# Kernel tuning notes

Hardware: AMD Instinct MI355X
Metric: run time of the kernel (lower is better)

The kernel has to match this reference:

```python
import jax, jax.numpy as jnp
import numpy as np


def setup_inputs() -> dict:
    key = jax.random.key(0)
    k1, k2, k3 = jax.random.split(key, 3)
    D, L, BATCH = 768, 8192, 4
    h = jax.random.normal(k1, (D, L), dtype=jnp.float32)
    x = jax.random.normal(k2, (BATCH, D, L), dtype=jnp.float32)
    B = jax.random.normal(k3, (D, 1), dtype=jnp.float32)
    return {"h": h, "x": x, "B": B}


def reference(h, x, B):
    # FFT-based long convolution (Hyena FFTConv) with residual term x * B.
    L = h.shape[-1]
    n = 2 * L  # zero-pad to 2L for linear (non-circular) convolution
    # torch.fft.rfft(..., norm='forward') divides by n; x uses default (backward, no scale);
    # torch.fft.irfft(..., norm='forward') multiplies by n. jnp supports the same norm args.
    h_f = jnp.fft.rfft(h, n=n, norm="forward")          # [D, L+1] complex
    x_f = jnp.fft.rfft(x, n=n)                            # [BATCH, D, L+1] complex
    y = jnp.fft.irfft(h_f * x_f, n=n, norm="forward")[..., :L]  # [BATCH, D, L]
    y = y + x * B  # residual with per-channel gain, B broadcasts over L
    return y.astype(h.dtype)
```

## Files before the change

kernel.cpp:

```cpp
#include <hip/hip_runtime.h>

#define DCH   768
#define NHALF 8192
#define NTH   512
#define PHYS(i) ((i) + ((i) >> 4))
#define LDSE  (NHALF + NHALF / 16)
#define NFULL 16384
#define NTH2  1024
#define LDSE2 (NFULL + NFULL / 16)

#define C1F 0.9238795325112867f
#define S1F 0.3826834323650898f
#define C2F 0.7071067811865476f

typedef float v2f __attribute__((ext_vector_type(2)));

__device__ __forceinline__ v2f mk(float x, float y) { v2f r; r.x = x; r.y = y; return r; }
__device__ __forceinline__ v2f cmul(v2f a, v2f b) {
    v2f re = a.xx * b;
    return __builtin_elementwise_fma(mk(-a.y, a.y), mk(b.y, b.x), re);
}
__device__ __forceinline__ v2f mnegi(v2f t) { return mk(t.y, -t.x); }
__device__ __forceinline__ v2f wtw(float rev) {
    return mk(__builtin_amdgcn_cosf(rev), __builtin_amdgcn_sinf(rev));
}
__device__ __forceinline__ int drev8(int v) {
    return ((v & 3) << 6) | ((v & 12) << 2) | ((v >> 2) & 12) | ((v >> 6) & 3);
}
__device__ __forceinline__ constexpr int rev2i(int a) { return ((a & 3) << 2) | ((a >> 2) & 3); }
__device__ __forceinline__ constexpr int rtof(int t)  { return ((t & 3) << 2) | (t >> 2); }

__device__ __forceinline__ v2f Ktw(int rt) {
    const float KC[16] = {1.0f, 0.980785280f, 0.923879533f, 0.831469612f,
                          0.707106781f, 0.555570233f, 0.382683432f, 0.195090322f,
                          0.0f, -0.195090322f, -0.382683432f, -0.555570233f,
                          -0.707106781f, -0.831469612f, -0.923879533f, -0.980785280f};
    const float KS[16] = {0.0f, -0.195090322f, -0.382683432f, -0.555570233f,
                          -0.707106781f, -0.831469612f, -0.923879533f, -0.980785280f,
                          -1.0f, -0.980785280f, -0.923879533f, -0.831469612f,
                          -0.707106781f, -0.555570233f, -0.382683432f, -0.195090322f};
    return mk(KC[rt], KS[rt]);
}

__device__ __forceinline__ void dif16(v2f* a, float r1) {
    const v2f w10 = wtw(r1);
    const v2f sq  = cmul(w10, w10);
    const v2f cu  = cmul(sq, w10);
#pragma unroll
    for (int ai = 0; ai < 4; ++ai) {
        v2f w1, w2, w3;
        if (ai == 0)      { w1 = w10; w2 = sq; w3 = cu; }
        else if (ai == 1) { w1 = cmul(w10, mk(C1F, -S1F));
                            w2 = cmul(sq,  mk(C2F, -C2F));
                            w3 = cmul(cu,  mk(S1F, -C1F)); }
        else if (ai == 2) { w1 = cmul(w10, mk(C2F, -C2F));
                            w2 = mk(sq.y, -sq.x);
                            w3 = cmul(cu,  mk(-C2F, -C2F)); }
        else              { w1 = cmul(w10, mk(S1F, -C1F));
                            w2 = cmul(sq,  mk(-C2F, -C2F));
                            w3 = cmul(cu,  mk(-C1F,  S1F)); }
        v2f u0 = a[ai], u1 = a[ai + 4], u2 = a[ai + 8], u3 = a[ai + 12];
        v2f t0 = u0 + u2, t1 = u1 + u3;
        v2f t2 = u0 - u2, t3 = u1 - u3;
        v2f mi3 = mnegi(t3);
        a[ai]      = t0 + t1;
        a[ai + 4]  = cmul(t2 + mi3, w1);
        a[ai + 8]  = cmul(t0 - t1, w2);
        a[ai + 12] = cmul(t2 - mi3, w3);
    }
    const v2f v1 = cmul(sq, sq);
    const v2f v2 = cmul(v1, v1);
    const v2f v3 = cmul(v2, v1);
#pragma unroll
    for (int p = 0; p < 4; ++p) {
        v2f u0 = a[4 * p], u1 = a[4 * p + 1], u2 = a[4 * p + 2], u3 = a[4 * p + 3];
        v2f t0 = u0 + u2, t1 = u1 + u3;
        v2f t2 = u0 - u2, t3 = u1 - u3;
        v2f mi3 = mnegi(t3);
        a[4 * p]     = t0 + t1;
        a[4 * p + 1] = cmul(t2 + mi3, v1);
        a[4 * p + 2] = cmul(t0 - t1, v2);
        a[4 * p + 3] = cmul(t2 - mi3, v3);
    }
}
__device__ __forceinline__ void dit16(v2f* a, float r1) {
    const v2f w10 = wtw(r1);
    const v2f sq  = cmul(w10, w10);
    const v2f cu  = cmul(sq, w10);
    const v2f v1  = cmul(sq, sq);
    const v2f v2  = cmul(v1, v1);
    const v2f v3  = cmul(v2, v1);
#pragma unroll
    for (int p = 0; p < 4; ++p) {
        v2f b0 = a[4 * p];
        v2f b1 = cmul(a[4 * p + 1], v1);
        v2f b2 = cmul(a[4 * p + 2], v2);
        v2f b3 = cmul(a[4 * p + 3], v3);
        v2f t0 = b0 + b2, t1 = b0 - b2;
        v2f t2 = b1 + b3;
        v2f dd = b3 - b1;
        v2f t3 = mnegi(dd);
        a[4 * p]     = t0 + t2;
        a[4 * p + 1] = t1 + t3;
        a[4 * p + 2] = t0 - t2;
        a[4 * p + 3] = t1 - t3;
    }
#pragma unroll
    for (int ai = 0; ai < 4; ++ai) {
        v2f w1, w2, w3;
        if (ai == 0)      { w1 = w10; w2 = sq; w3 = cu; }
        else if (ai == 1) { w1 = cmul(w10, mk(C1F, S1F));
                            w2 = cmul(sq,  mk(C2F, C2F));
                            w3 = cmul(cu,  mk(S1F, C1F)); }
        else if (ai == 2) { w1 = cmul(w10, mk(C2F, C2F));
                            w2 = mk(-sq.y, sq.x);
                            w3 = cmul(cu,  mk(-C2F, C2F)); }
        else              { w1 = cmul(w10, mk(S1F, C1F));
                            w2 = cmul(sq,  mk(-C2F, C2F));
                            w3 = cmul(cu,  mk(-C1F, -S1F)); }
        v2f b0 = a[ai];
        v2f b1 = cmul(a[ai + 4], w1);
        v2f b2 = cmul(a[ai + 8], w2);
        v2f b3 = cmul(a[ai + 12], w3);
        v2f t0 = b0 + b2, t1 = b0 - b2;
        v2f t2 = b1 + b3;
        v2f dd = b3 - b1;
        v2f t3 = mnegi(dd);
        a[ai]      = t0 + t2;
        a[ai + 4]  = t1 + t3;
        a[ai + 8]  = t0 - t2;
        a[ai + 12] = t1 - t3;
    }
}
__device__ __forceinline__ void fwd4x4(v2f* a) {
#pragma unroll
    for (int u = 0; u < 4; ++u) {
        v2f u0 = a[4*u], u1 = a[4*u+1], u2 = a[4*u+2], u3 = a[4*u+3];
        v2f t0 = u0 + u2, t1 = u1 + u3, t2 = u0 - u2, t3 = u1 - u3;
        v2f mi3 = mnegi(t3);
        a[4*u] = t0 + t1; a[4*u+1] = t2 + mi3;
        a[4*u+2] = t0 - t1; a[4*u+3] = t2 - mi3;
    }
}
__device__ __forceinline__ void inv4x4(v2f* a) {
#pragma unroll
    for (int u = 0; u < 4; ++u) {
        v2f b0 = a[4*u], b1 = a[4*u+1], b2 = a[4*u+2], b3 = a[4*u+3];
        v2f t0 = b0 + b2, t1 = b0 - b2, t2 = b1 + b3;
        v2f dd = b3 - b1;
        v2f t3 = mnegi(dd);
        a[4*u] = t0 + t2; a[4*u+1] = t1 + t3;
        a[4*u+2] = t0 - t2; a[4*u+3] = t1 - t3;
    }
}

__device__ __forceinline__ void fwd8k(const v2f* __restrict__ src,
                                      v2f* __restrict__ z, const int w, v2f* a) {
    const float R2 = 0.70710678118654752f;
#pragma unroll
    for (int g = 0; g < 2; ++g) {
        const int i0 = w + 512 * g;
        v2f c0 = src[i0], c1 = src[i0 + 1024], c2 = src[i0 + 2048], c3 = src[i0 + 3072];
        const v2f wA  = wtw(-(float)i0 * (1.0f / 8192.0f));
        const v2f wB  = cmul(wA, wA);
        const v2f wB2 = cmul(wB, wB);
        const v2f wB3 = cmul(wB2, wB);
        const int pb = PHYS(i0);
        v2f t0 = c0 + c2, t1 = c1 + c3, t2 = c0 - c2, t3 = c1 - c3;
        v2f mi3 = mnegi(t3);
        z[pb]            = t0 + t1;
        z[pb + 1088]     = cmul(t2 + mi3, wB);
        z[pb + 2 * 1088] = cmul(t0 - t1, wB2);
        z[pb + 3 * 1088] = cmul(t2 - mi3, wB3);
        v2f d0 = cmul(c0, wA);
        v2f d1 = cmul(c1, cmul(wA, mk(R2, -R2)));
        v2f d2 = cmul(c2, mk(wA.y, -wA.x));
        v2f d3 = cmul(c3, cmul(wA, mk(-R2, -R2)));
        t0 = d0 + d2; t1 = d1 + d3; t2 = d0 - d2; t3 = d1 - d3;
        mi3 = mnegi(t3);
        z[pb + 4 * 1088] = t0 + t1;
        z[pb + 5 * 1088] = cmul(t2 + mi3, wB);
        z[pb + 6 * 1088] = cmul(t0 - t1, wB2);
        z[pb + 7 * 1088] = cmul(t2 - mi3, wB3);
    }
    __syncthreads();
    {
        const int j = w & 63, blk = w >> 6;
        const int base = PHYS(blk * 1024 + j);
#pragma unroll
        for (int t = 0; t < 16; ++t) a[t] = z[base + 68 * t];
        dif16(a, -(float)j * (1.0f / 1024.0f));
#pragma unroll
        for (int t = 0; t < 16; ++t) z[base + 68 * t] = a[t];
    }
    __syncthreads();
    {
        const int j = w & 3, g = w >> 2;
        const int i0 = g * 64 + j;
#pragma unroll
        for (int t = 0; t < 16; ++t) a[t] = z[PHYS(i0 + 4 * t)];
        dif16(a, -(float)j * (1.0f / 64.0f));
#pragma unroll
        for (int t = 0; t < 16; ++t) z[PHYS(i0 + 4 * t)] = a[t];
    }
    __syncthreads();
    {
        const int base = 17 * w;
#pragma unroll
        for (int t = 0; t < 16; ++t) a[t] = z[base + t];
        fwd4x4(a);
#pragma unroll
        for (int t = 0; t < 16; ++t) z[base + t] = a[t];
    }
    __syncthreads();
}

extern "C" __global__ void __launch_bounds__(NTH, 4)
hspec_kernel(const float* __restrict__ hg, const float* __restrict__ bg,
             float* __restrict__ wsHf, float* __restrict__ wsNy) {
    extern __shared__ v2f z[];
    const int w = threadIdx.x;
    const int d = blockIdx.x;
    const v2f* hr = (const v2f*)hg + (size_t)d * 4096;
    v2f a[16];
    fwd8k(hr, z, w, a);

    const float Bd = bg[d];
    const float invN = 1.0f / 16384.0f;
    v2f* out = (v2f*)wsHf + (size_t)d * NHALF;
    const int wm = w & 255, whi = w >> 8;
    const int k0 = 2 * drev8(wm) + whi;
    const v2f wk0 = wtw(-(float)k0 * (1.0f / 16384.0f));
    int qm = 0;
    if (w != 0) { const int bq = (512 - k0) >> 1; qm = (whi << 8) | drev8(bq); }
#pragma unroll
    for (int t = 0; t < 16; ++t) {
        const int rt = rtof(t);
        if (w == 0 && t == 0) {
            v2f C0 = a[0];
            out[0] = mk((C0.x + C0.y + Bd) * invN, 0.0f);
            ((v2f*)wsNy)[d] = mk((C0.x - C0.y + Bd) * invN, 0.0f);
        } else {
            const int cq = (w == 0) ? rev2i(16 - rt) : rev2i(15 - rt);
            const v2f Cq = z[17 * qm + cq];
            const v2f Cp = a[t];
            const v2f cA = mk(0.5f * (Cp.x + Cq.x), 0.5f * (Cp.y - Cq.y));
            const v2f cB = mk(0.5f * (Cp.y + Cq.y), -0.5f * (Cp.x - Cq.x));
            const v2f Wk = cmul(wk0, Ktw(rt));
            const v2f Hf = cA + cmul(Wk, cB);
            out[(t << 9) + w] = mk((Hf.x + Bd) * invN, Hf.y * invN);
        }
    }
}

extern "C" __global__ void __launch_bounds__(NTH, 4)
fftconv_main(const float* __restrict__ xg, const float* __restrict__ wsHf,
             const float* __restrict__ wsNy, float* __restrict__ yg) {
    extern __shared__ v2f z[];
    const int w = threadIdx.x;
    const int bid = blockIdx.x;
    const int d = bid >> 2, b = bid & 3;
    const v2f* xr = (const v2f*)xg + (size_t)(b * DCH + d) * 4096;
    const v2f* hrow = (const v2f*)wsHf + (size_t)d * NHALF;
    const float R2 = 0.70710678118654752f;
    v2f a[16];
    fwd8k(xr, z, w, a);

    {
        const int wm = w & 255, whi = w >> 8;
        const int k0 = 2 * drev8(wm) + whi;
        const v2f wk0 = wtw(-(float)k0 * (1.0f / 16384.0f));
        int qm = 0;
        if (w != 0) { const int bq = (512 - k0) >> 1; qm = (whi << 8) | drev8(bq); }
#pragma unroll
        for (int t = 0; t < 16; ++t) {
            if ((t & 3) > 1) continue;
            const int rt = rtof(t);
            if (w == 0 && t == 0) {
                v2f C0 = a[0];
                float X0 = C0.x + C0.y, XN = C0.x - C0.y;
                v2f H0 = hrow[0];
                v2f HN = ((const v2f*)wsNy)[d];
                v2f Y1 = mk(X0 * H0.x, X0 * H0.y);
                v2f Y2 = mk(XN * HN.x, XN * HN.y);
                v2f S  = mk(Y1.x + Y2.x, Y1.y - Y2.y);
                v2f Dd = mk(Y1.x - Y2.x, Y1.y + Y2.y);
                a[0] = mk(S.x - Dd.y, S.y + Dd.x);
            } else {
                const int cq = (w == 0) ? rev2i(16 - rt) : rev2i(15 - rt);
                const v2f Cq = z[17 * qm + cq];
                const v2f Cp = a[t];
                const v2f cA = mk(0.5f * (Cp.x + Cq.x), 0.5f * (Cp.y - Cq.y));
                const v2f cB = mk(0.5f * (Cp.y + Cq.y), -0.5f * (Cp.x - Cq.x));
                const v2f Wk = cmul(wk0, Ktw(rt));
                const v2f T  = cmul(Wk, cB);
                const v2f X1 = cA + T;
                const v2f X2 = mk(cA.x - T.x, -(cA.y - T.y));
                const v2f Hp = hrow[(t << 9) + w];
                const v2f Hq = hrow[(cq << 9) + qm];
                const v2f Y1 = cmul(X1, Hp);
                const v2f Y2 = cmul(X2, Hq);
                const v2f S  = mk(Y1.x + Y2.x, Y1.y - Y2.y);
                const v2f Dd = mk(Y1.x - Y2.x, Y1.y + Y2.y);
                const v2f Vk = mk(Wk.x, -Wk.y);
                const v2f U  = cmul(Vk, Dd);
                a[t]            = mk(S.x - U.y, S.y + U.x);
                z[17 * qm + cq] = mk(S.x + U.y, U.x - S.y);
            }
        }
        if (w == 0) {
            const v2f Cp = z[2];
            const v2f cA = mk(Cp.x, 0.0f);
            const v2f cB = mk(Cp.y, 0.0f);
            const v2f Wk = mk(0.0f, -1.0f);
            const v2f T  = cmul(Wk, cB);
            const v2f X1 = cA + T;
            const v2f X2 = mk(cA.x - T.x, -(cA.y - T.y));
            const v2f Hp = hrow[(2 << 9)];
            const v2f Y1 = cmul(X1, Hp);
            const v2f Y2 = cmul(X2, Hp);
            const v2f S  = mk(Y1.x + Y2.x, Y1.y - Y2.y);
            const v2f Dd = mk(Y1.x - Y2.x, Y1.y + Y2.y);
            const v2f Vk = mk(0.0f, 1.0f);
            const v2f U  = cmul(Vk, Dd);
            z[2] = mk(S.x - U.y, S.y + U.x);
        }
    }
    __syncthreads();
    {
        const int base = 17 * w;
#pragma unroll
        for (int t = 0; t < 16; ++t)
            if ((t & 3) > 1) a[t] = z[base + t];
        inv4x4(a);
#pragma unroll
        for (int t = 0; t < 16; ++t) z[base + t] = a[t];
    }
    __syncthreads();
    {
        const int j = w & 3, g = w >> 2;
        const int i0 = g * 64 + j;
#pragma unroll
        for (int t = 0; t < 16; ++t) a[t] = z[PHYS(i0 + 4 * t)];
        dit16(a, (float)j * (1.0f / 64.0f));
#pragma unroll
        for (int t = 0; t < 16; ++t) z[PHYS(i0 + 4 * t)] = a[t];
    }
    __syncthreads();
    {
        const int j = w & 63, blk = w >> 6;
        const int base = PHYS(blk * 1024 + j);
#pragma unroll
        for (int t = 0; t < 16; ++t) a[t] = z[base + 68 * t];
        dit16(a, (float)j * (1.0f / 1024.0f));
#pragma unroll
        for (int t = 0; t < 16; ++t) z[base + 68 * t] = a[t];
    }
    __syncthreads();
    {
        v2f* yr = (v2f*)yg + (size_t)(b * DCH + d) * 4096;
#pragma unroll
        for (int g = 0; g < 2; ++g) {
            const int i0 = w + 512 * g;
            const int pb = PHYS(i0);
            v2f q0 = z[pb],            q1 = z[pb + 1088],
                q2 = z[pb + 2 * 1088], q3 = z[pb + 3 * 1088],
                q4 = z[pb + 4 * 1088], q5 = z[pb + 5 * 1088],
                q6 = z[pb + 6 * 1088], q7 = z[pb + 7 * 1088];
            const v2f vA  = wtw((float)i0 * (1.0f / 8192.0f));
            const v2f vB  = cmul(vA, vA);
            const v2f vB2 = cmul(vB, vB);
            const v2f vB3 = cmul(vB2, vB);
            v2f b1 = cmul(q1, vB), b2 = cmul(q2, vB2), b3 = cmul(q3, vB3);
            v2f t0 = q0 + b2, t1 = q0 - b2, t2 = b1 + b3;
            v2f dd = b3 - b1;
            v2f t3 = mnegi(dd);
            v2f T0 = t0 + t2, T1 = t1 + t3, T2 = t0 - t2, T3 = t1 - t3;
            b1 = cmul(q5, vB); b2 = cmul(q6, vB2); b3 = cmul(q7, vB3);
            t0 = q4 + b2; t1 = q4 - b2; t2 = b1 + b3;
            dd = b3 - b1;
            t3 = mnegi(dd);
            v2f B0 = t0 + t2, B1 = t1 + t3, B2 = t0 - t2, B3 = t1 - t3;
            yr[i0]        = T0 + cmul(B0, vA);
            yr[i0 + 1024] = T1 + cmul(B1, cmul(vA, mk(R2, R2)));
            yr[i0 + 2048] = T2 + cmul(B2, mk(-vA.y, vA.x));
            yr[i0 + 3072] = T3 + cmul(B3, cmul(vA, mk(-R2, R2)));
        }
    }
}

__device__ __forceinline__ int drev14(int v) {
    int r = 0;
#pragma unroll
    for (int i = 0; i < 7; ++i) { r = (r << 2) | (v & 3); v >>= 2; }
    return r;
}
__device__ __forceinline__ int drev10(int v) {
    int r = 0;
#pragma unroll
    for (int i = 0; i < 5; ++i) { r = (r << 2) | (v & 3); v >>= 2; }
    return r;
}

extern "C" __global__ void __launch_bounds__(NTH2, 4)
fftconv_v2(const float* __restrict__ hg, const float* __restrict__ xg,
           const float* __restrict__ bg, float* __restrict__ yg) {
    extern __shared__ v2f z[];
    const int w = threadIdx.x;
    const int bid = blockIdx.x;
    const int d = bid >> 2, b = bid & 3;
    const float* xr = xg + (size_t)(b * DCH + d) * 8192;
    const float* hr = hg + (size_t)d * 8192;
    v2f a[16];
    float xv[8];
    {
#pragma unroll
        for (int t = 0; t < 8; ++t) {
            xv[t] = xr[w + 1024 * t];
            float hv = hr[w + 1024 * t];
            a[t] = mk(xv[t], hv);
        }
        const float r1 = -(float)w * (1.0f / 16384.0f);
#pragma unroll
        for (int ai = 0; ai < 4; ++ai) {
            v2f u0 = a[ai], u1 = a[ai + 4];
            v2f mi3 = mk(u1.y, -u1.x);
            v2f w1 = wtw(r1 - 0.0625f * ai);
            v2f w2 = cmul(w1, w1), w3 = cmul(w2, w1);
            a[ai]      = u0 + u1;
            a[ai + 4]  = cmul(u0 + mi3, w1);
            a[ai + 8]  = cmul(u0 - u1, w2);
            a[ai + 12] = cmul(u0 - mi3, w3);
        }
        v2f v1 = wtw(4.0f * r1);
        v2f v2 = cmul(v1, v1), v3 = cmul(v2, v1);
#pragma unroll
        for (int p = 0; p < 4; ++p) {
            v2f u0 = a[4 * p], u1 = a[4 * p + 1], u2 = a[4 * p + 2], u3 = a[4 * p + 3];
            v2f t0 = u0 + u2, t1 = u1 + u3;
            v2f t2 = u0 - u2, t3 = u1 - u3;
            v2f mi3 = mnegi(t3);
            a[4 * p]     = t0 + t1;
            a[4 * p + 1] = cmul(t2 + mi3, v1);
            a[4 * p + 2] = cmul(t0 - t1, v2);
            a[4 * p + 3] = cmul(t2 - mi3, v3);
        }
        const int base = PHYS(w);
#pragma unroll
        for (int t = 0; t < 16; ++t) z[base + 1088 * t] = a[t];
    }
    __syncthreads();
    {
        const int j = w & 63, grp = w >> 6;
        const int base = PHYS(grp * 1024 + j);
#pragma unroll
        for (int t = 0; t < 16; ++t) a[t] = z[base + 68 * t];
        dif16(a, -(float)j * (1.0f / 1024.0f));
#pragma unroll
        for (int t = 0; t < 16; ++t) z[base + 68 * t] = a[t];
    }
    __syncthreads();
    {
        const int j = w & 3, grp = w >> 2;
        const int i0 = grp * 64 + j;
#pragma unroll
        for (int t = 0; t < 16; ++t) a[t] = z[PHYS(i0 + 4 * t)];
        dif16(a, -(float)j * (1.0f / 64.0f));
#pragma unroll
        for (int t = 0; t < 16; ++t) z[PHYS(i0 + 4 * t)] = a[t];
    }
    __syncthreads();
    {
        const int base = 17 * w;
#pragma unroll
        for (int t = 0; t < 16; ++t) a[t] = z[base + t];
        fwd4x4(a);
#pragma unroll
        for (int t = 0; t < 16; ++t) z[base + t] = a[t];
        __syncthreads();
        const int kw = drev10(w);
#pragma unroll
        for (int t = 0; t < 16; ++t) {
            const int rt = (((t & 3) << 2) | (t >> 2));
            const int k = (rt << 10) | kw;
            const int pp = drev14(16384 - k);
            const v2f Zm = z[PHYS(pp)];
            const v2f Zp = a[t];
            const v2f A  = mk(Zp.x + Zm.x, Zp.y - Zm.y);
            const v2f Dv = mk(Zp.x - Zm.x, Zp.y + Zm.y);
            const v2f X  = mk(0.5f * A.x, 0.5f * A.y);
            const v2f H  = mk(0.5f * Dv.y, -0.5f * Dv.x);
            a[t] = cmul(X, H);
        }
        __syncthreads();
        inv4x4(a);
#pragma unroll
        for (int t = 0; t < 16; ++t) z[base + t] = a[t];
    }
    __syncthreads();
    {
        const int j = w & 3, grp = w >> 2;
        const int i0 = grp * 64 + j;
#pragma unroll
        for (int t = 0; t < 16; ++t) a[t] = z[PHYS(i0 + 4 * t)];
        dit16(a, (float)j * (1.0f / 64.0f));
#pragma unroll
        for (int t = 0; t < 16; ++t) z[PHYS(i0 + 4 * t)] = a[t];
    }
    __syncthreads();
    {
        const int j = w & 63, grp = w >> 6;
        const int base = PHYS(grp * 1024 + j);
#pragma unroll
        for (int t = 0; t < 16; ++t) a[t] = z[base + 68 * t];
        dit16(a, (float)j * (1.0f / 1024.0f));
#pragma unroll
        for (int t = 0; t < 16; ++t) z[base + 68 * t] = a[t];
    }
    __syncthreads();
    {
        const int base = PHYS(w);
#pragma unroll
        for (int t = 0; t < 16; ++t) a[t] = z[base + 1088 * t];
        const float r1 = (float)w * (1.0f / 16384.0f);
        v2f v1 = wtw(4.0f * r1);
        v2f v2 = cmul(v1, v1), v3 = cmul(v2, v1);
#pragma unroll
        for (int p = 0; p < 4; ++p) {
            v2f b0 = a[4 * p];
            v2f b1 = cmul(a[4 * p + 1], v1);
            v2f b2 = cmul(a[4 * p + 2], v2);
            v2f b3 = cmul(a[4 * p + 3], v3);
            v2f t0 = b0 + b2, t1 = b0 - b2;
            v2f t2 = b1 + b3;
            v2f dd = b3 - b1;
            v2f t3 = mnegi(dd);
            a[4 * p]     = t0 + t2;
            a[4 * p + 1] = t1 + t3;
            a[4 * p + 2] = t0 - t2;
            a[4 * p + 3] = t1 - t3;
        }
        const float bd = bg[d];
        const float invN = 1.0f / 16384.0f;
#pragma unroll
        for (int ai = 0; ai < 4; ++ai) {
            v2f w1 = wtw(r1 + 0.0625f * ai);
            v2f w2 = cmul(w1, w1), w3 = cmul(w2, w1);
            v2f b0 = a[ai];
            v2f vv1 = cmul(a[ai + 4], w1);
            v2f vv2 = cmul(a[ai + 8], w2);
            v2f vv3 = cmul(a[ai + 12], w3);
            v2f t0 = b0 + vv2, t1 = b0 - vv2;
            v2f t2 = vv1 + vv3;
            v2f dd = vv3 - vv1;
            v2f t3 = mnegi(dd);
            v2f o0 = t0 + t2;
            v2f o1 = t1 + t3;
            yg[(size_t)(b * DCH + d) * 8192 + w + 1024 * ai]        = fmaf(xv[ai], bd, o0.x * invN);
            yg[(size_t)(b * DCH + d) * 8192 + w + 4096 + 1024 * ai] = fmaf(xv[ai + 4], bd, o1.x * invN);
        }
    }
}

extern "C" void kernel_launch(void* const* d_in, const int* in_sizes, int n_in,
                              void* d_out, int out_size, void* d_ws, size_t ws_size,
                              hipStream_t stream) {
    (void)in_sizes; (void)n_in; (void)out_size;
    const float* h = (const float*)d_in[0];
    const float* x = (const float*)d_in[1];
    const float* B = (const float*)d_in[2];
    float* y = (float*)d_out;

    const size_t need = (size_t)(DCH * NHALF + DCH) * sizeof(float2);
    if (ws_size >= need && d_ws != nullptr) {
        (void)hipFuncSetAttribute((const void*)hspec_kernel,
                                  hipFuncAttributeMaxDynamicSharedMemorySize,
                                  LDSE * (int)sizeof(float2));
        (void)hipFuncSetAttribute((const void*)fftconv_main,
                                  hipFuncAttributeMaxDynamicSharedMemorySize,
                                  LDSE * (int)sizeof(float2));
        float* wsHf = (float*)d_ws;
        float* wsNy = wsHf + 2 * (size_t)DCH * NHALF;
        hspec_kernel<<<dim3(DCH), dim3(NTH), LDSE * sizeof(float2), stream>>>(h, B, wsHf, wsNy);
        fftconv_main<<<dim3(4 * DCH), dim3(NTH), LDSE * sizeof(float2), stream>>>(x, wsHf, wsNy, y);
    } else {
        (void)hipFuncSetAttribute((const void*)fftconv_v2,
                                  hipFuncAttributeMaxDynamicSharedMemorySize,
                                  LDSE2 * (int)sizeof(float2));
        fftconv_v2<<<dim3(4 * DCH), dim3(NTH2), LDSE2 * sizeof(float2), stream>>>(h, x, B, y);
    }
}
```

Measured before the change: 132.0 us.

## Prefetch x and H spectrum into registers before forward FFT, skip dead LDS stores

Global loads of the x row and of the H spectrum values needed in the pointwise stage are issued up front into registers, pinned with empty asm so they overlap the forward FFT instead of stalling afterwards. The last forward stage skips LDS stores for elements that stay in registers. The per-group twiddle for g=1 is now a complex multiply by a constant rather than a second sin/cos evaluation. The cost is higher register pressure under the 4-blocks launch bound, which may cause spills.

New measurement: 134.7 us. 2.0% more time.

```diff
diff --git a/kernel.cpp b/kernel.cpp
--- a/kernel.cpp
+++ b/kernel.cpp
@@ -154,14 +154,16 @@
     }
 }
 
-__device__ __forceinline__ void fwd8k(const v2f* __restrict__ src,
-                                      v2f* __restrict__ z, const int w, v2f* a) {
+template<bool PUB8>
+__device__ __forceinline__ void fwd8k_body(const v2f* __restrict__ c,
+                                           v2f* __restrict__ z, const int w, v2f* a) {
     const float R2 = 0.70710678118654752f;
+    const v2f wA0 = wtw(-(float)w * (1.0f / 8192.0f));
 #pragma unroll
     for (int g = 0; g < 2; ++g) {
         const int i0 = w + 512 * g;
-        v2f c0 = src[i0], c1 = src[i0 + 1024], c2 = src[i0 + 2048], c3 = src[i0 + 3072];
-        const v2f wA  = wtw(-(float)i0 * (1.0f / 8192.0f));
+        v2f c0 = c[4*g], c1 = c[4*g+1], c2 = c[4*g+2], c3 = c[4*g+3];
+        const v2f wA  = (g == 0) ? wA0 : cmul(wA0, mk(C1F, -S1F));
         const v2f wB  = cmul(wA, wA);
         const v2f wB2 = cmul(wB, wB);
         const v2f wB3 = cmul(wB2, wB);
@@ -210,7 +212,8 @@
         for (int t = 0; t < 16; ++t) a[t] = z[base + t];
         fwd4x4(a);
 #pragma unroll
-        for (int t = 0; t < 16; ++t) z[base + t] = a[t];
+        for (int t = 0; t < 16; ++t)
+            if (!PUB8 || (t & 3) > 1) z[base + t] = a[t];
     }
     __syncthreads();
 }
@@ -222,8 +225,12 @@
     const int w = threadIdx.x;
     const int d = blockIdx.x;
     const v2f* hr = (const v2f*)hg + (size_t)d * 4096;
-    v2f a[16];
-    fwd8k(hr, z, w, a);
+    v2f a[16], c[8];
+#pragma unroll
+    for (int g = 0; g < 2; ++g)
+#pragma unroll
+        for (int t = 0; t < 4; ++t) c[4*g + t] = hr[w + 512*g + 1024*t];
+    fwd8k_body<false>(c, z, w, a);
 
     const float Bd = bg[d];
     const float invN = 1.0f / 16384.0f;
@@ -263,15 +270,37 @@
     const v2f* xr = (const v2f*)xg + (size_t)(b * DCH + d) * 4096;
     const v2f* hrow = (const v2f*)wsHf + (size_t)d * NHALF;
     const float R2 = 0.70710678118654752f;
-    v2f a[16];
-    fwd8k(xr, z, w, a);
-
-    {
-        const int wm = w & 255, whi = w >> 8;
-        const int k0 = 2 * drev8(wm) + whi;
+    v2f a[16], c[8];
+
+#pragma unroll
+    for (int g = 0; g < 2; ++g)
+#pragma unroll
+        for (int t = 0; t < 4; ++t) c[4*g + t] = xr[w + 512*g + 1024*t];
+
+    const int wm = w & 255, whi = w >> 8;
+    const int k0 = 2 * drev8(wm) + whi;
+    int qm = 0;
+    if (w != 0) { const int bq = (512 - k0) >> 1; qm = (whi << 8) | drev8(bq); }
+    v2f hp[8], hq[8];
+#pragma unroll
+    for (int u = 0; u < 8; ++u) {
+        const int t = ((u >> 1) << 2) | (u & 1);
+        const int rt = rtof(t);
+        const int cq = (w == 0) ? rev2i(16 - rt) : rev2i(15 - rt);
+        hp[u] = hrow[(t << 9) + w];
+        hq[u] = hrow[(cq << 9) + qm];
+    }
+    v2f hn = ((const v2f*)wsNy)[d];
+    asm volatile("" :: "v"(hp[0]), "v"(hp[1]), "v"(hp[2]), "v"(hp[3]),
+                       "v"(hp[4]), "v"(hp[5]), "v"(hp[6]), "v"(hp[7]));
+    asm volatile("" :: "v"(hq[0]), "v"(hq[1]), "v"(hq[2]), "v"(hq[3]),
+                       "v"(hq[4]), "v"(hq[5]), "v"(hq[6]), "v"(hq[7]), "v"(hn));
+
+    fwd8k_body<true>(c, z, w, a);
+
+    {
         const v2f wk0 = wtw(-(float)k0 * (1.0f / 16384.0f));
-        int qm = 0;
-        if (w != 0) { const int bq = (512 - k0) >> 1; qm = (whi << 8) | drev8(bq); }
+        int u = 0;
 #pragma unroll
         for (int t = 0; t < 16; ++t) {
             if ((t & 3) > 1) continue;
@@ -279,10 +308,8 @@
             if (w == 0 && t == 0) {
                 v2f C0 = a[0];
                 float X0 = C0.x + C0.y, XN = C0.x - C0.y;
-                v2f H0 = hrow[0];
-                v2f HN = ((const v2f*)wsNy)[d];
-                v2f Y1 = mk(X0 * H0.x, X0 * H0.y);
-                v2f Y2 = mk(XN * HN.x, XN * HN.y);
+                v2f Y1 = mk(X0 * hp[0].x, X0 * hp[0].y);
+                v2f Y2 = mk(XN * hn.x, XN * hn.y);
                 v2f S  = mk(Y1.x + Y2.x, Y1.y - Y2.y);
                 v2f Dd = mk(Y1.x - Y2.x, Y1.y + Y2.y);
                 a[0] = mk(S.x - Dd.y, S.y + Dd.x);
@@ -296,10 +323,8 @@
                 const v2f T  = cmul(Wk, cB);
                 const v2f X1 = cA + T;
                 const v2f X2 = mk(cA.x - T.x, -(cA.y - T.y));
-                const v2f Hp = hrow[(t << 9) + w];
-                const v2f Hq = hrow[(cq << 9) + qm];
-                const v2f Y1 = cmul(X1, Hp);
-                const v2f Y2 = cmul(X2, Hq);
+                const v2f Y1 = cmul(X1, hp[u]);
+                const v2f Y2 = cmul(X2, hq[u]);
                 const v2f S  = mk(Y1.x + Y2.x, Y1.y - Y2.y);
                 const v2f Dd = mk(Y1.x - Y2.x, Y1.y + Y2.y);
                 const v2f Vk = mk(Wk.x, -Wk.y);
@@ -307,6 +332,7 @@
                 a[t]            = mk(S.x - U.y, S.y + U.x);
                 z[17 * qm + cq] = mk(S.x + U.y, U.x - S.y);
             }
+            ++u;
         }
         if (w == 0) {
             const v2f Cp = z[2];
@@ -359,6 +385,7 @@
     __syncthreads();
     {
         v2f* yr = (v2f*)yg + (size_t)(b * DCH + d) * 4096;
+        const v2f vA0 = wtw((float)w * (1.0f / 8192.0f));
 #pragma unroll
         for (int g = 0; g < 2; ++g) {
             const int i0 = w + 512 * g;
@@ -367,7 +394,7 @@
                 q2 = z[pb + 2 * 1088], q3 = z[pb + 3 * 1088],
                 q4 = z[pb + 4 * 1088], q5 = z[pb + 5 * 1088],
                 q6 = z[pb + 6 * 1088], q7 = z[pb + 7 * 1088];
-            const v2f vA  = wtw((float)i0 * (1.0f / 8192.0f));
+            const v2f vA  = (g == 0) ? vA0 : cmul(vA0, mk(C1F, S1F));
             const v2f vB  = cmul(vA, vA);
             const v2f vB2 = cmul(vB, vB);
             const v2f vB3 = cmul(vB2, vB);
```
